# Kernel tuning notes

Measured on AMD Instinct MI355X. Metric: run time of the kernel, lower is better.

Reference implementation:

```python
import math
import jax, jax.numpy as jnp
import numpy as np

B, T, C = 4, 2048, 1024

def setup_inputs() -> dict:
    key = jax.random.key(0)
    k1, k2 = jax.random.split(key)
    x = jax.random.normal(k1, (B, T, C), dtype=jnp.float32)
    W_kqv = jax.random.normal(k2, (C, 3 * C), dtype=jnp.float32) * 0.02
    return {"x": x, "W_kqv": W_kqv}

def reference(x, W_kqv):
    Bq, Tq, Cq = x.shape
    qkv = jnp.einsum('btc,cd->btd', x, W_kqv)            # [B,T,3C]
    q, k, v = jnp.split(qkv, 3, axis=2)                   # each [B,T,C]
    # scaled scores: note scale is 1/sqrt(n_embed), matching the source
    attn = jnp.einsum('btc,bsc->bts', q, k) / math.sqrt(Cq)  # [B,T,T]
    mask = jnp.tril(jnp.ones((Tq, Tq), dtype=bool))
    attn = jnp.where(mask, attn, -jnp.inf)
    attn = jax.nn.softmax(attn, axis=-1)
    y = jnp.einsum('bts,bsc->btc', attn, v)               # [B,T,C]
    return y
```

## Files before the change

### kernel.cpp

```cpp
#include <hip/hip_runtime.h>

typedef unsigned short u16;
typedef __bf16 bf16x8 __attribute__((ext_vector_type(8)));
typedef float f32x4 __attribute__((ext_vector_type(4)));

#define Bb 4
#define Tt 2048
#define Cc 1024

#define GLOAD_LDS16(g, l)                                                     \
  __builtin_amdgcn_global_load_lds(                                           \
      (const __attribute__((address_space(1))) void*)(g),                     \
      (__attribute__((address_space(3))) void*)(l), 16, 0, 0)

#define WAITV8 asm volatile("s_waitcnt vmcnt(8)" ::: "memory")
#define WAITV0 asm volatile("s_waitcnt vmcnt(0)" ::: "memory")

__device__ inline u16 f2bf(float f) {
  unsigned u = __builtin_bit_cast(unsigned, f);
  unsigned r = u + 0x7fffu + ((u >> 16) & 1u);
  return (u16)(r >> 16);
}

__global__ __launch_bounds__(256) void cast_f32_bf16_vec4(
    const float* __restrict__ in, u16* __restrict__ out, int n4) {
  int i = blockIdx.x * 256 + threadIdx.x;
  if (i >= n4) return;
  float4 v = reinterpret_cast<const float4*>(in)[i];
  ushort4 o;
  o.x = f2bf(v.x); o.y = f2bf(v.y); o.z = f2bf(v.z); o.w = f2bf(v.w);
  reinterpret_cast<ushort4*>(out)[i] = o;
}

__global__ __launch_bounds__(256) void zero_f32(float* __restrict__ p, int n) {
  int i = blockIdx.x * 256 + threadIdx.x;
  if (i < n) p[i] = 0.f;
}

__global__ __launch_bounds__(256) void transpose_cast_w(
    const float* __restrict__ W, u16* __restrict__ Wt) {
  __shared__ float tile[32][33];
  int n0 = blockIdx.x * 32;
  int k0 = blockIdx.y * 32;
  int tx = threadIdx.x;
  int ty = threadIdx.y;
#pragma unroll
  for (int i = 0; i < 4; i++)
    tile[ty + i * 8][tx] = W[(size_t)(k0 + ty + i * 8) * 3072 + n0 + tx];
  __syncthreads();
#pragma unroll
  for (int i = 0; i < 4; i++)
    Wt[(size_t)(n0 + ty + i * 8) * 1024 + k0 + tx] = f2bf(tile[tx][ty + i * 8]);
}


__device__ __forceinline__ void stage_unit(const u16* __restrict__ G, int ld,
                                           u16* lds_unit, int tid) {
#pragma unroll
  for (int j = 0; j < 2; j++) {
    int u = j * 8192 + tid * 16;
    int l = u ^ (((u >> 7) & 7) << 4);
    int grow = l >> 6;
    int gcol = (l & 63) >> 1;
    GLOAD_LDS16(G + (size_t)grow * ld + gcol, lds_unit + (u >> 1));
  }
}

__device__ __forceinline__ bf16x8 lds_frag(const u16* unit, int row, int fq) {
  int off = row * 64 + fq * 16;
  off ^= ((off >> 7) & 7) << 4;
  return *reinterpret_cast<const bf16x8*>(
      reinterpret_cast<const char*>(unit) + off);
}

template <int MODE>
__global__ __launch_bounds__(512, 2) void gemm256(
    const u16* __restrict__ A0, const u16* __restrict__ B0,
    size_t sAbatch, size_t sBbatch,
    u16* __restrict__ qO, u16* __restrict__ kO, u16* __restrict__ vTO,
    u16* __restrict__ EO, float* __restrict__ rowsum) {
  const int lda = Cc, ldb = Cc, NT = Cc / 64;
  int bx = blockIdx.x, by = blockIdx.y, bz = blockIdx.z;
  if (MODE == 1 && bx > by) return;

  const u16* A = A0 + (size_t)bz * sAbatch + (size_t)by * 256 * lda;
  const u16* Bt = B0 + (size_t)bz * sBbatch + (size_t)bx * 256 * ldb;

  __shared__ __attribute__((aligned(16))) u16 lds[4][2][8192];

  int tid = threadIdx.x;
  int lane = tid & 63, w = tid >> 6;
  int wm = (w >> 2) * 128, wn = (w & 3) * 64;
  int fr = lane & 15, fq = lane >> 4;

  f32x4 acc[8][4] = {};

  stage_unit(A + 0, lda, &lds[0][0][0], tid);
  stage_unit(Bt + 0, ldb, &lds[2][0][0], tid);
  stage_unit(A + 32, lda, &lds[1][0][0], tid);
  stage_unit(Bt + 32, ldb, &lds[3][0][0], tid);
  stage_unit(A + 64, lda, &lds[0][1][0], tid);
  stage_unit(Bt + 64, ldb, &lds[2][1][0], tid);
  WAITV8;
  __builtin_amdgcn_s_barrier();

  for (int t = 0; t < NT; ++t) {
    int par = t & 1;
    int parn = par ^ 1;
    bool st1 = (t + 1 < NT);
    bool st2 = (t + 2 < NT);
    bool tail = (t >= NT - 2);
    bf16x8 a[4], b[4];

#pragma unroll
    for (int mi = 0; mi < 4; mi++)
      a[mi] = lds_frag(&lds[0][par][0], wm + mi * 16 + fr, fq);
#pragma unroll
    for (int ni = 0; ni < 4; ni++)
      b[ni] = lds_frag(&lds[2][par][0], wn + ni * 16 + fr, fq);
    if (st1) stage_unit(A + (t + 1) * 64 + 32, lda, &lds[1][parn][0], tid);
    __builtin_amdgcn_s_barrier();
    __builtin_amdgcn_s_setprio(1);
#pragma unroll
    for (int mi = 0; mi < 4; mi++)
#pragma unroll
      for (int ni = 0; ni < 4; ni++)
        acc[mi][ni] = __builtin_amdgcn_mfma_f32_16x16x32_bf16(a[mi], b[ni], acc[mi][ni], 0, 0, 0);
    __builtin_amdgcn_s_setprio(0);
    __builtin_amdgcn_s_barrier();

#pragma unroll
    for (int mi = 0; mi < 4; mi++)
      a[mi] = lds_frag(&lds[0][par][0], wm + 64 + mi * 16 + fr, fq);
    if (st1) stage_unit(Bt + (t + 1) * 64 + 32, ldb, &lds[3][parn][0], tid);
    __builtin_amdgcn_s_barrier();
    __builtin_amdgcn_s_setprio(1);
#pragma unroll
    for (int mi = 0; mi < 4; mi++)
#pragma unroll
      for (int ni = 0; ni < 4; ni++)
        acc[4 + mi][ni] = __builtin_amdgcn_mfma_f32_16x16x32_bf16(a[mi], b[ni], acc[4 + mi][ni], 0, 0, 0);
    __builtin_amdgcn_s_setprio(0);
    if (tail) { WAITV0; } else { WAITV8; }
    __builtin_amdgcn_s_barrier();

#pragma unroll
    for (int mi = 0; mi < 4; mi++)
      a[mi] = lds_frag(&lds[1][par][0], wm + mi * 16 + fr, fq);
#pragma unroll
    for (int ni = 0; ni < 4; ni++)
      b[ni] = lds_frag(&lds[3][par][0], wn + ni * 16 + fr, fq);
    if (st2) stage_unit(A + (t + 2) * 64, lda, &lds[0][par][0], tid);
    __builtin_amdgcn_s_barrier();
    __builtin_amdgcn_s_setprio(1);
#pragma unroll
    for (int mi = 0; mi < 4; mi++)
#pragma unroll
      for (int ni = 0; ni < 4; ni++)
        acc[mi][ni] = __builtin_amdgcn_mfma_f32_16x16x32_bf16(a[mi], b[ni], acc[mi][ni], 0, 0, 0);
    __builtin_amdgcn_s_setprio(0);
    __builtin_amdgcn_s_barrier();

#pragma unroll
    for (int mi = 0; mi < 4; mi++)
      a[mi] = lds_frag(&lds[1][par][0], wm + 64 + mi * 16 + fr, fq);
    if (st2) stage_unit(Bt + (t + 2) * 64, ldb, &lds[2][par][0], tid);
    __builtin_amdgcn_s_barrier();
    __builtin_amdgcn_s_setprio(1);
#pragma unroll
    for (int mi = 0; mi < 4; mi++)
#pragma unroll
      for (int ni = 0; ni < 4; ni++)
        acc[4 + mi][ni] = __builtin_amdgcn_mfma_f32_16x16x32_bf16(a[mi], b[ni], acc[4 + mi][ni], 0, 0, 0);
    __builtin_amdgcn_s_setprio(0);
    if (tail) { WAITV0; } else { WAITV8; }
    __builtin_amdgcn_s_barrier();
  }

  if (MODE == 0) {
#pragma unroll
    for (int mi = 0; mi < 8; mi++) {
#pragma unroll
      for (int ni = 0; ni < 4; ni++) {
#pragma unroll
        for (int r = 0; r < 4; r++) {
          int m = by * 256 + wm + mi * 16 + fq * 4 + r;
          int n = bx * 256 + wn + ni * 16 + fr;
          u16 hv = f2bf(acc[mi][ni][r]);
          int seg = n >> 10, cn = n & 1023;
          int b = m >> 11, tt = m & 2047;
          if (seg == 0)
            qO[(((size_t)(b * Tt + tt)) << 10) + cn] = hv;
          else if (seg == 1)
            kO[(((size_t)(b * Tt + tt)) << 10) + cn] = hv;
          else
            vTO[((size_t)(b * Cc + cn)) * Tt + tt] = hv;
        }
      }
    }
  } else {
    float rpart[8][4];
#pragma unroll
    for (int mi = 0; mi < 8; mi++)
#pragma unroll
      for (int r = 0; r < 4; r++) rpart[mi][r] = 0.f;
#pragma unroll
    for (int mi = 0; mi < 8; mi++) {
#pragma unroll
      for (int ni = 0; ni < 4; ni++) {
#pragma unroll
        for (int r = 0; r < 4; r++) {
          int m = by * 256 + wm + mi * 16 + fq * 4 + r;
          int n = bx * 256 + wn + ni * 16 + fr;
          float e = 0.f;
          if (n <= m) e = __expf(fminf(acc[mi][ni][r] * 0.03125f, 30.f));
          EO[((size_t)bz * Tt + m) * Tt + n] = f2bf(e);
          rpart[mi][r] += e;
        }
      }
    }
#pragma unroll
    for (int mi = 0; mi < 8; mi++) {
#pragma unroll
      for (int r = 0; r < 4; r++) {
        float v = rpart[mi][r];
        v += __shfl_xor(v, 1);
        v += __shfl_xor(v, 2);
        v += __shfl_xor(v, 4);
        v += __shfl_xor(v, 8);
        if (fr == 0) {
          int m = by * 256 + wm + mi * 16 + fq * 4 + r;
          atomicAdd(&rowsum[(size_t)bz * Tt + m], v);
        }
      }
    }
  }
}

__global__ __launch_bounds__(256) void gemm_bt_pv(
    const u16* __restrict__ A0, const u16* __restrict__ B0,
    size_t sAbatch, size_t sBbatch,
    int K, int lda, int ldb, const float* __restrict__ rowsum,
    float* __restrict__ YO) {
  int bx = blockIdx.x, by = blockIdx.y, bz = blockIdx.z;

  const u16* A = A0 + (size_t)bz * sAbatch + (size_t)by * 128 * lda;
  const u16* Bt = B0 + (size_t)bz * sBbatch + (size_t)bx * 128 * ldb;
  int kEnd = min(K, (by + 1) * 128);

  __shared__ __attribute__((aligned(16))) u16 As[128 * 32];
  __shared__ __attribute__((aligned(16))) u16 Bs[128 * 32];

  int tid = threadIdx.x;
  int lane = tid & 63, w = tid >> 6;
  int wr = (w >> 1) * 64, wc = (w & 1) * 64;
  int row16 = lane & 15, kq = (lane >> 4) * 8;

  int r0 = w * 16 + (lane >> 2);
  int c0 = (lane & 3) * 8;

  f32x4 acc[4][4] = {};

  for (int kt = 0; kt < kEnd; kt += 32) {
    const u16* Ag = A + (size_t)r0 * lda + kt + c0;
    const u16* Bg = Bt + (size_t)r0 * ldb + kt + c0;
    GLOAD_LDS16(Ag, &As[w * 512]);
    GLOAD_LDS16(Ag + (size_t)64 * lda, &As[2048 + w * 512]);
    GLOAD_LDS16(Bg, &Bs[w * 512]);
    GLOAD_LDS16(Bg + (size_t)64 * ldb, &Bs[2048 + w * 512]);
    __syncthreads();

    bf16x8 a[4], b[4];
#pragma unroll
    for (int m = 0; m < 4; m++)
      a[m] = *reinterpret_cast<const bf16x8*>(&As[(wr + m * 16 + row16) * 32 + kq]);
#pragma unroll
    for (int n = 0; n < 4; n++)
      b[n] = *reinterpret_cast<const bf16x8*>(&Bs[(wc + n * 16 + row16) * 32 + kq]);
#pragma unroll
    for (int m = 0; m < 4; m++)
#pragma unroll
      for (int n = 0; n < 4; n++)
        acc[m][n] = __builtin_amdgcn_mfma_f32_16x16x32_bf16(a[m], b[n], acc[m][n], 0, 0, 0);
    __syncthreads();
  }

  int colf = lane & 15, rbase = (lane >> 4) * 4;
#pragma unroll
  for (int i = 0; i < 4; i++) {
#pragma unroll
    for (int r = 0; r < 4; r++) {
      int m = by * 128 + wr + i * 16 + rbase + r;
      float inv = 1.0f / rowsum[(size_t)bz * Tt + m];
#pragma unroll
      for (int j = 0; j < 4; j++) {
        int n = bx * 128 + wc + j * 16 + colf;
        YO[((size_t)bz * Tt + m) * Cc + n] = acc[i][j][r] * inv;
      }
    }
  }
}

extern "C" void kernel_launch(void* const* d_in, const int* in_sizes, int n_in,
                              void* d_out, int out_size, void* d_ws, size_t ws_size,
                              hipStream_t stream) {
  const float* x = (const float*)d_in[0];
  const float* W = (const float*)d_in[1];
  float* Y = (float*)d_out;

  char* ws = (char*)d_ws;
  size_t off = 0;
  auto carve = [&](size_t bytes) -> void* {
    void* p = ws + off;
    off += (bytes + 255) & ~(size_t)255;
    return p;
  };
  u16* xb = (u16*)carve((size_t)Bb * Tt * Cc * 2);
  u16* wt = (u16*)carve((size_t)3 * Cc * Cc * 2);
  u16* qb = (u16*)carve((size_t)Bb * Tt * Cc * 2);
  u16* kb = (u16*)carve((size_t)Bb * Tt * Cc * 2);
  u16* vT = (u16*)carve((size_t)Bb * Cc * Tt * 2);
  u16* E = (u16*)carve((size_t)Bb * Tt * Tt * 2);
  float* rowsum = (float*)carve((size_t)Bb * Tt * 4);

  cast_f32_bf16_vec4<<<(Bb * Tt * Cc / 4 + 255) / 256, 256, 0, stream>>>(
      x, xb, Bb * Tt * Cc / 4);
  zero_f32<<<(Bb * Tt + 255) / 256, 256, 0, stream>>>(rowsum, Bb * Tt);
  transpose_cast_w<<<dim3(96, 32), dim3(32, 8), 0, stream>>>(W, wt);
  gemm256<0><<<dim3(12, 32, 1), 512, 0, stream>>>(
      xb, wt, 0, 0, qb, kb, vT, nullptr, nullptr);
  gemm256<1><<<dim3(8, 8, 4), 512, 0, stream>>>(
      qb, kb, (size_t)Tt * Cc, (size_t)Tt * Cc, nullptr, nullptr, nullptr, E, rowsum);
  gemm_bt_pv<<<dim3(8, 16, 4), 256, 0, stream>>>(
      E, vT, (size_t)Tt * Tt, (size_t)Cc * Tt, Tt, Tt, Tt, rowsum, Y);
}
```

Baseline: 280.6 us.

## Replace QKV projection GEMM with dedicated 256x128 tile kernel

The QKV projection moves off the shared 256x256, 512-thread gemm256 kernel onto a new 256-thread kernel with 256x128 tiles, K-step 32 and a simple double buffer. This doubles the grid to 768 blocks, aiming for better load balance across the CUs, with up to 3 blocks per CU and less LDS per block. The trade-off is lower arithmetic intensity per tile and a less elaborate pipeline (a full vmcnt(0) wait each iteration). gemm256 is reduced to the attention-score mode only.

```diff
diff --git a/kernel.cpp b/kernel.cpp
--- a/kernel.cpp
+++ b/kernel.cpp
@@ -53,16 +53,13 @@
     Wt[(size_t)(n0 + ty + i * 8) * 1024 + k0 + tx] = f2bf(tile[tx][ty + i * 8]);
 }
 
-
 __device__ __forceinline__ void stage_unit(const u16* __restrict__ G, int ld,
                                            u16* lds_unit, int tid) {
 #pragma unroll
   for (int j = 0; j < 2; j++) {
     int u = j * 8192 + tid * 16;
     int l = u ^ (((u >> 7) & 7) << 4);
-    int grow = l >> 6;
-    int gcol = (l & 63) >> 1;
-    GLOAD_LDS16(G + (size_t)grow * ld + gcol, lds_unit + (u >> 1));
+    GLOAD_LDS16(G + (size_t)(l >> 6) * ld + ((l & 63) >> 1), lds_unit + (u >> 1));
   }
 }
 
@@ -73,11 +70,108 @@
       reinterpret_cast<const char*>(unit) + off);
 }
 
+__device__ __forceinline__ void stageA256(const u16* __restrict__ G,
+                                          u16* unit, int tid) {
+#pragma unroll
+  for (int j = 0; j < 4; j++) {
+    int u = j * 4096 + tid * 16;
+    int l = u ^ (((u >> 7) & 7) << 4);
+    GLOAD_LDS16(G + (size_t)(l >> 6) * Cc + ((l & 63) >> 1), unit + (u >> 1));
+  }
+}
+__device__ __forceinline__ void stageB256(const u16* __restrict__ G,
+                                          u16* unit, int tid) {
+#pragma unroll
+  for (int j = 0; j < 2; j++) {
+    int u = j * 4096 + tid * 16;
+    int l = u ^ (((u >> 7) & 7) << 4);
+    GLOAD_LDS16(G + (size_t)(l >> 6) * Cc + ((l & 63) >> 1), unit + (u >> 1));
+  }
+}
+
+__global__ __launch_bounds__(256, 3) void gemm_qkv_256x128(
+    const u16* __restrict__ A0, const u16* __restrict__ B0,
+    u16* __restrict__ qO, u16* __restrict__ kO, u16* __restrict__ vTO) {
+  const int NT = Cc / 32;
+  int bx = blockIdx.x, by = blockIdx.y;
+  const u16* A = A0 + (size_t)by * 256 * Cc;
+  const u16* Bt = B0 + (size_t)bx * 128 * Cc;
+
+  __shared__ __attribute__((aligned(16))) u16 ldsA[2][8192];
+  __shared__ __attribute__((aligned(16))) u16 ldsB[2][4096];
+
+  int tid = threadIdx.x;
+  int lane = tid & 63, w = tid >> 6;
+  int wm = (w >> 1) * 128, wn = (w & 1) * 64;
+  int fr = lane & 15, fq = lane >> 4;
+
+  f32x4 acc[8][4] = {};
+
+  stageA256(A, ldsA[0], tid);
+  stageB256(Bt, ldsB[0], tid);
+  WAITV0;
+  __builtin_amdgcn_s_barrier();
+
+  for (int t = 0; t < NT; ++t) {
+    int par = t & 1, parn = par ^ 1;
+    if (t + 1 < NT) {
+      stageA256(A + (t + 1) * 32, ldsA[parn], tid);
+      stageB256(Bt + (t + 1) * 32, ldsB[parn], tid);
+    }
+    bf16x8 a[4], b[4];
+#pragma unroll
+    for (int ni = 0; ni < 4; ni++)
+      b[ni] = lds_frag(ldsB[par], wn + ni * 16 + fr, fq);
+#pragma unroll
+    for (int mi = 0; mi < 4; mi++)
+      a[mi] = lds_frag(ldsA[par], wm + mi * 16 + fr, fq);
+    __builtin_amdgcn_s_setprio(1);
+#pragma unroll
+    for (int mi = 0; mi < 4; mi++)
+#pragma unroll
+      for (int ni = 0; ni < 4; ni++)
+        acc[mi][ni] = __builtin_amdgcn_mfma_f32_16x16x32_bf16(a[mi], b[ni], acc[mi][ni], 0, 0, 0);
+    __builtin_amdgcn_s_setprio(0);
+#pragma unroll
+    for (int mi = 0; mi < 4; mi++)
+      a[mi] = lds_frag(ldsA[par], wm + 64 + mi * 16 + fr, fq);
+    __builtin_amdgcn_s_setprio(1);
+#pragma unroll
+    for (int mi = 0; mi < 4; mi++)
+#pragma unroll
+      for (int ni = 0; ni < 4; ni++)
+        acc[4 + mi][ni] = __builtin_amdgcn_mfma_f32_16x16x32_bf16(a[mi], b[ni], acc[4 + mi][ni], 0, 0, 0);
+    __builtin_amdgcn_s_setprio(0);
+    if (t + 1 < NT) WAITV0;
+    __builtin_amdgcn_s_barrier();
+  }
+
+#pragma unroll
+  for (int mi = 0; mi < 8; mi++) {
+#pragma unroll
+    for (int ni = 0; ni < 4; ni++) {
+#pragma unroll
+      for (int r = 0; r < 4; r++) {
+        int m = by * 256 + wm + mi * 16 + fq * 4 + r;
+        int n = bx * 128 + wn + ni * 16 + fr;
+        u16 hv = f2bf(acc[mi][ni][r]);
+        int seg = n >> 10, cn = n & 1023;
+        int b = m >> 11, tt = m & 2047;
+        if (seg == 0)
+          qO[(((size_t)(b * Tt + tt)) << 10) + cn] = hv;
+        else if (seg == 1)
+          kO[(((size_t)(b * Tt + tt)) << 10) + cn] = hv;
+        else
+          vTO[((size_t)(b * Cc + cn)) * Tt + tt] = hv;
+      }
+    }
+  }
+}
+
 template <int MODE>
 __global__ __launch_bounds__(512, 2) void gemm256(
     const u16* __restrict__ A0, const u16* __restrict__ B0,
     size_t sAbatch, size_t sBbatch,
-    u16* __restrict__ qO, u16* __restrict__ kO, u16* __restrict__ vTO,
     u16* __restrict__ EO, float* __restrict__ rowsum) {
   const int lda = Cc, ldb = Cc, NT = Cc / 64;
   int bx = blockIdx.x, by = blockIdx.y, bz = blockIdx.z;
@@ -177,28 +271,7 @@
     __builtin_amdgcn_s_barrier();
   }
 
-  if (MODE == 0) {
-#pragma unroll
-    for (int mi = 0; mi < 8; mi++) {
-#pragma unroll
-      for (int ni = 0; ni < 4; ni++) {
-#pragma unroll
-        for (int r = 0; r < 4; r++) {
-          int m = by * 256 + wm + mi * 16 + fq * 4 + r;
-          int n = bx * 256 + wn + ni * 16 + fr;
-          u16 hv = f2bf(acc[mi][ni][r]);
-          int seg = n >> 10, cn = n & 1023;
-          int b = m >> 11, tt = m & 2047;
-          if (seg == 0)
-            qO[(((size_t)(b * Tt + tt)) << 10) + cn] = hv;
-          else if (seg == 1)
-            kO[(((size_t)(b * Tt + tt)) << 10) + cn] = hv;
-          else
-            vTO[((size_t)(b * Cc + cn)) * Tt + tt] = hv;
-        }
-      }
-    }
-  } else {
+  {
     float rpart[8][4];
 #pragma unroll
     for (int mi = 0; mi < 8; mi++)
@@ -327,10 +400,9 @@
       x, xb, Bb * Tt * Cc / 4);
   zero_f32<<<(Bb * Tt + 255) / 256, 256, 0, stream>>>(rowsum, Bb * Tt);
   transpose_cast_w<<<dim3(96, 32), dim3(32, 8), 0, stream>>>(W, wt);
-  gemm256<0><<<dim3(12, 32, 1), 512, 0, stream>>>(
-      xb, wt, 0, 0, qb, kb, vT, nullptr, nullptr);
+  gemm_qkv_256x128<<<dim3(24, 32), 256, 0, stream>>>(xb, wt, qb, kb, vT);
   gemm256<1><<<dim3(8, 8, 4), 512, 0, stream>>>(
-      qb, kb, (size_t)Tt * Cc, (size_t)Tt * Cc, nullptr, nullptr, nullptr, E, rowsum);
+      qb, kb, (size_t)Tt * Cc, (size_t)Tt * Cc, E, rowsum);
   gemm_bt_pv<<<dim3(8, 16, 4), 256, 0, stream>>>(
       E, vT, (size_t)Tt * Tt, (size_t)Cc * Tt, Tt, Tt, Tt, rowsum, Y);
 }
```

New measurement: 306.7 us. 9.3% more time.
